# Performance work log

Measured on AMD Instinct MI355X. Metric: run time of the kernel, lower is better.

Reference implementation:

```python
import jax, jax.numpy as jnp
import numpy as np

B, T = 64, 512
N_EMB, HIDDEN, VOCAB = 768, 256, 3072


def setup_inputs() -> dict:
    key = jax.random.key(0)
    ks = jax.random.split(key, 5)
    def xavier(k, shape):
        bound = float(np.sqrt(6.0 / (shape[0] + shape[1])))
        return jax.random.uniform(k, shape, jnp.float32, -bound, bound)
    return {
        "idx": jax.random.randint(ks[0], (B, T), 0, VOCAB),
        "emb_table": jax.random.normal(ks[1], (VOCAB, N_EMB), jnp.float32),
        "Wxh": xavier(ks[2], (N_EMB, HIDDEN)),
        "Whh": xavier(ks[3], (HIDDEN, HIDDEN)),
        "Wy": xavier(ks[4], (HIDDEN, VOCAB)),
        "By": jnp.zeros((VOCAB,), jnp.float32),
        "Bh": jnp.zeros((HIDDEN,), jnp.float32),
    }


def reference(idx, emb_table, Wxh, Whh, Wy, By, Bh):
    # embedded: [B, T, E] -> scan over time with hidden carry [B, H]
    embedded = emb_table[idx]                      # gather
    xWxh = jnp.einsum('bte,eh->tbh', embedded, Wxh)  # precompute input projection

    def step(hidden, x_t):
        hidden = jnp.tanh(x_t + hidden @ Whh + Bh)
        return hidden, None

    h0 = jnp.zeros((idx.shape[0], Whh.shape[0]), embedded.dtype)
    hidden, _ = jax.lax.scan(step, h0, xWxh)
    # return_sequences=False: only the last step's output is returned
    out = hidden @ Wy + By
    return out, hidden
```

## Files before the change

### kernel.cpp

```cpp
#include <hip/hip_runtime.h>
#include <hip/hip_bf16.h>

typedef _Float16 half8 __attribute__((ext_vector_type(8)));
typedef float f32x4 __attribute__((ext_vector_type(4)));

#define B_SZ 64
#define T_SZ 512
#define E_SZ 768
#define H_SZ 256
#define V_SZ 3072

#define WS_P     0u
#define WS_WT    16777216u
#define WS_WF    17170432u

static __device__ __forceinline__ float fast_tanh(float x) {
  float e = __builtin_amdgcn_exp2f(x * 2.8853900817779268f);
  return 1.0f - 2.0f * __builtin_amdgcn_rcpf(1.0f + e);
}

__global__ __launch_bounds__(256) void k0_convert(
    const float* __restrict__ Wxh,
    const float* __restrict__ Whh,
    _Float16* __restrict__ Wtf,
    _Float16* __restrict__ Wf)
{
  int gid = blockIdx.x * 256 + threadIdx.x;
  if (gid < E_SZ * H_SZ) {
    int e = gid >> 8, n = gid & 255;
    float v = Wxh[gid];
    int ki = e >> 5, kb = (e >> 3) & 3, j = e & 7;
    int f  = ((n >> 4) << 6) | (kb << 4) | (n & 15);
    Wtf[(size_t)ki * 8192 + (size_t)f * 8 + j] = (_Float16)v;
  }
  if (gid < 65536) {
    int row = gid >> 8, col = gid & 255;
    float v = Whh[gid];
    int kt = row >> 5, quad = (row >> 3) & 3, j = row & 7;
    int nt = col >> 4;
    int lane = (quad << 4) | (col & 15);
    Wf[(((size_t)(nt * 8 + kt) * 64 + lane) * 8) + j] = (_Float16)v;
  }
}

__global__ __launch_bounds__(256) void k1_xproj(
    const float* __restrict__ emb,
    const _Float16* __restrict__ Wtf,
    _Float16* __restrict__ P)
{
  const int tid  = threadIdx.x;
  const int w    = tid >> 6;
  const int lane = tid & 63;
  const int m16  = lane & 15;
  const int quad = lane >> 4;
  const int r = blockIdx.x * 64 + w * 16 + m16;
  const float* Arow = emb + (size_t)r * E_SZ + quad * 8;

  __shared__ __align__(16) _Float16 bp[2][16 * 64 * 8];
  uint4 stg[4];
#pragma unroll
  for (int pp = 0; pp < 4; ++pp)
    stg[pp] = *(const uint4*)(Wtf + (size_t)(tid + 256 * pp) * 8);
  f32x4 af0 = *(const f32x4*)(Arow);
  f32x4 af1 = *(const f32x4*)(Arow + 4);

  f32x4 acc[16];
#pragma unroll
  for (int n = 0; n < 16; ++n) { f32x4 z = {0.f, 0.f, 0.f, 0.f}; acc[n] = z; }

#pragma unroll
  for (int pp = 0; pp < 4; ++pp)
    *(uint4*)(bp[0] + (size_t)(tid + 256 * pp) * 8) = stg[pp];
  __syncthreads();

#pragma unroll 1
  for (int ki = 0; ki < 24; ++ki) {
    const _Float16* cur = bp[ki & 1];
    f32x4 af0n = af0, af1n = af1;
    if (ki < 23) {
#pragma unroll
      for (int pp = 0; pp < 4; ++pp)
        stg[pp] = *(const uint4*)(Wtf + (size_t)(ki + 1) * 8192
                                      + (size_t)(tid + 256 * pp) * 8);
      af0n = *(const f32x4*)(Arow + (ki + 1) * 32);
      af1n = *(const f32x4*)(Arow + (ki + 1) * 32 + 4);
    }
    half8 a;
#pragma unroll
    for (int e = 0; e < 4; ++e) { a[e] = (_Float16)af0[e]; a[4 + e] = (_Float16)af1[e]; }
#pragma unroll
    for (int nt = 0; nt < 16; ++nt) {
      half8 bb = *(const half8*)(cur + (size_t)(nt * 64 + lane) * 8);
      acc[nt] = __builtin_amdgcn_mfma_f32_16x16x32_f16(a, bb, acc[nt], 0, 0, 0);
    }
    if (ki < 23) {
#pragma unroll
      for (int pp = 0; pp < 4; ++pp)
        *(uint4*)(bp[(ki + 1) & 1] + (size_t)(tid + 256 * pp) * 8) = stg[pp];
      __syncthreads();
    }
    af0 = af0n; af1 = af1n;
  }
  const int rbase = blockIdx.x * 64 + w * 16 + quad * 4;
#pragma unroll
  for (int nt = 0; nt < 16; ++nt) {
    const int col = nt * 16 + m16;
#pragma unroll
    for (int rg = 0; rg < 4; ++rg) {
      P[(size_t)(rbase + rg) * H_SZ + col] = (_Float16)acc[nt][rg];
    }
  }
}

#define LDFRAG(C, KT, R0, R1, R2, R3) { \
  uint4 q = Wf4[(((size_t)(w * 4 + C) * 8 + KT) * 64) + lane]; \
  asm volatile("v_accvgpr_write_b32 a" #R0 ", %0" :: "v"(q.x) : "a" #R0); \
  asm volatile("v_accvgpr_write_b32 a" #R1 ", %0" :: "v"(q.y) : "a" #R1); \
  asm volatile("v_accvgpr_write_b32 a" #R2 ", %0" :: "v"(q.z) : "a" #R2); \
  asm volatile("v_accvgpr_write_b32 a" #R3 ", %0" :: "v"(q.w) : "a" #R3); }

#define MFMA_K0(A0, Z) \
  asm volatile( \
    "v_mfma_f32_16x16x32_f16 %[t0], %[a], a[0:3],   %[z]\n\t" \
    "v_mfma_f32_16x16x32_f16 %[t1], %[a], a[32:35], %[z]\n\t" \
    "v_mfma_f32_16x16x32_f16 %[t2], %[a], a[64:67], %[z]\n\t" \
    "v_mfma_f32_16x16x32_f16 %[t3], %[a], a[96:99], %[z]" \
    : [t0] "=&v"(acc0), [t1] "=&v"(acc1), [t2] "=&v"(acc2), [t3] "=&v"(acc3) \
    : [a] "v"(A0), [z] "v"(Z));

#define MFMA_KT(A0, B0, B1, B2, B3) \
  asm volatile( \
    "v_mfma_f32_16x16x32_f16 %[t0], %[a], a[" #B0 "], %[t0]\n\t" \
    "v_mfma_f32_16x16x32_f16 %[t1], %[a], a[" #B1 "], %[t1]\n\t" \
    "v_mfma_f32_16x16x32_f16 %[t2], %[a], a[" #B2 "], %[t2]\n\t" \
    "v_mfma_f32_16x16x32_f16 %[t3], %[a], a[" #B3 "], %[t3]" \
    : [t0] "+v"(acc0), [t1] "+v"(acc1), [t2] "+v"(acc2), [t3] "+v"(acc3) \
    : [a] "v"(A0));

#define MFMA_K7(A0, B0, B1, B2, B3) \
  asm volatile( \
    "v_mfma_f32_16x16x32_f16 %[t0], %[a], a[" #B0 "], %[t0]\n\t" \
    "v_mfma_f32_16x16x32_f16 %[t1], %[a], a[" #B1 "], %[t1]\n\t" \
    "v_mfma_f32_16x16x32_f16 %[t2], %[a], a[" #B2 "], %[t2]\n\t" \
    "v_mfma_f32_16x16x32_f16 %[t3], %[a], a[" #B3 "], %[t3]\n\t" \
    "s_nop 7\n\t" \
    "s_nop 7" \
    : [t0] "+v"(acc0), [t1] "+v"(acc1), [t2] "+v"(acc2), [t3] "+v"(acc3) \
    : [a] "v"(A0));

__global__ __launch_bounds__(256) void k2_rnn(
    const _Float16* __restrict__ Wf,
    const _Float16* __restrict__ P,
    const int* __restrict__ idx,
    const float* __restrict__ Bh,
    const float* __restrict__ Wy,
    const float* __restrict__ By,
    float* __restrict__ out,
    float* __restrict__ hidout)
{
  const int b    = blockIdx.x;
  const int tid  = threadIdx.x;
  const int w    = tid >> 6;
  const int lane = tid & 63;
  const int quad = lane >> 4;
  __shared__ __align__(16) _Float16 hb[2][H_SZ];
  __shared__ int   ids[520];
  __shared__ float hf[H_SZ];
  const uint4* Wf4 = (const uint4*)Wf;

  LDFRAG(0,0,  0,  1,  2,  3)  LDFRAG(0,1,  4,  5,  6,  7)
  LDFRAG(0,2,  8,  9, 10, 11)  LDFRAG(0,3, 12, 13, 14, 15)
  LDFRAG(0,4, 16, 17, 18, 19)  LDFRAG(0,5, 20, 21, 22, 23)
  LDFRAG(0,6, 24, 25, 26, 27)  LDFRAG(0,7, 28, 29, 30, 31)
  LDFRAG(1,0, 32, 33, 34, 35)  LDFRAG(1,1, 36, 37, 38, 39)
  LDFRAG(1,2, 40, 41, 42, 43)  LDFRAG(1,3, 44, 45, 46, 47)
  LDFRAG(1,4, 48, 49, 50, 51)  LDFRAG(1,5, 52, 53, 54, 55)
  LDFRAG(1,6, 56, 57, 58, 59)  LDFRAG(1,7, 60, 61, 62, 63)
  LDFRAG(2,0, 64, 65, 66, 67)  LDFRAG(2,1, 68, 69, 70, 71)
  LDFRAG(2,2, 72, 73, 74, 75)  LDFRAG(2,3, 76, 77, 78, 79)
  LDFRAG(2,4, 80, 81, 82, 83)  LDFRAG(2,5, 84, 85, 86, 87)
  LDFRAG(2,6, 88, 89, 90, 91)  LDFRAG(2,7, 92, 93, 94, 95)
  LDFRAG(3,0, 96, 97, 98, 99)  LDFRAG(3,1,100,101,102,103)
  LDFRAG(3,2,104,105,106,107)  LDFRAG(3,3,108,109,110,111)
  LDFRAG(3,4,112,113,114,115)  LDFRAG(3,5,116,117,118,119)
  LDFRAG(3,6,120,121,122,123)  LDFRAG(3,7,124,125,126,127)

  const float bhj = Bh[tid];
  const int* idxb = idx + b * T_SZ;
  for (int i = tid; i < 520; i += 256) ids[i] = idxb[i < 512 ? i : 511];
  int rowA = idxb[2];
  int rowB = idxb[3];
  _Float16 xA = P[(size_t)idxb[0] * H_SZ + tid];
  _Float16 xB = P[(size_t)idxb[1] * H_SZ + tid];
  f32x4 zero4 = {0.f, 0.f, 0.f, 0.f};
  asm volatile("" : "+v"(zero4));
  hb[1][tid] = (_Float16)0.f;
  float hval = 0.f;
  __syncthreads();

#define K2_STEP(HR, HW, XV)                                              \
  {                                                                      \
    const _Float16* hr = (HR);                                           \
    half8 va0 = *(const half8*)(hr +   0 + quad * 8);                    \
    half8 va1 = *(const half8*)(hr +  32 + quad * 8);                    \
    half8 va2 = *(const half8*)(hr +  64 + quad * 8);                    \
    half8 va3 = *(const half8*)(hr +  96 + quad * 8);                    \
    half8 va4 = *(const half8*)(hr + 128 + quad * 8);                    \
    half8 va5 = *(const half8*)(hr + 160 + quad * 8);                    \
    half8 va6 = *(const half8*)(hr + 192 + quad * 8);                    \
    half8 va7 = *(const half8*)(hr + 224 + quad * 8);                    \
    f32x4 acc0, acc1, acc2, acc3;                                        \
    MFMA_K0(va0, zero4)                                                  \
    MFMA_KT(va1,   4:7,  36:39,  68:71, 100:103)                         \
    MFMA_KT(va2,  8:11,  40:43,  72:75, 104:107)                         \
    MFMA_KT(va3, 12:15,  44:47,  76:79, 108:111)                         \
    MFMA_KT(va4, 16:19,  48:51,  80:83, 112:115)                         \
    MFMA_KT(va5, 20:23,  52:55,  84:87, 116:119)                         \
    MFMA_KT(va6, 24:27,  56:59,  88:91, 120:123)                         \
    MFMA_K7(va7, 28:31,  60:63,  92:95, 124:127)                         \
    float v0 = acc0[0], v1 = acc1[0], v2 = acc2[0], v3 = acc3[0];        \
    float ylo = (quad & 1) ? v1 : v0;                                    \
    float yhi = (quad & 1) ? v3 : v2;                                    \
    float y   = (quad & 2) ? yhi : ylo;          \
    hval = fast_tanh(y + (XV) + bhj);                                    \
    (HW)[tid] = (_Float16)hval;                                          \
    __syncthreads();                                                     \
  }

#pragma unroll 1
  for (int tt = 0; tt < 256; ++tt) {
    float xvA = (float)xA;
    xA = P[rowA * H_SZ + tid];
    rowA = ids[2 * tt + 4];
    K2_STEP(hb[1], hb[0], xvA)
    float xvB = (float)xB;
    xB = P[rowB * H_SZ + tid];
    rowB = ids[2 * tt + 5];
    K2_STEP(hb[0], hb[1], xvB)
  }
#undef K2_STEP
  hidout[b * H_SZ + tid] = hval;

  hf[tid] = hval;
  __syncthreads();
#pragma unroll 1
  for (int c = 0; c < 12; ++c) {
    const int v = c * 256 + tid;
    float a0 = By[v], a1 = 0.f, a2 = 0.f, a3 = 0.f;
#pragma unroll 4
    for (int jj = 0; jj < H_SZ; jj += 4) {
      a0 += hf[jj + 0] * Wy[(size_t)(jj + 0) * V_SZ + v];
      a1 += hf[jj + 1] * Wy[(size_t)(jj + 1) * V_SZ + v];
      a2 += hf[jj + 2] * Wy[(size_t)(jj + 2) * V_SZ + v];
      a3 += hf[jj + 3] * Wy[(size_t)(jj + 3) * V_SZ + v];
    }
    out[(size_t)b * V_SZ + v] = (a0 + a1) + (a2 + a3);
  }
}

extern "C" void kernel_launch(void* const* d_in, const int* in_sizes, int n_in,
                              void* d_out, int out_size, void* d_ws, size_t ws_size,
                              hipStream_t stream)
{
  const int*   idx = (const int*)d_in[0];
  const float* emb = (const float*)d_in[1];
  const float* Wxh = (const float*)d_in[2];
  const float* Whh = (const float*)d_in[3];
  const float* Wy  = (const float*)d_in[4];
  const float* By  = (const float*)d_in[5];
  const float* Bh  = (const float*)d_in[6];

  char* ws = (char*)d_ws;
  _Float16* P    = (_Float16*)(ws + WS_P);
  _Float16* Wtf  = (_Float16*)(ws + WS_WT);
  _Float16* Wf   = (_Float16*)(ws + WS_WF);

  float* out    = (float*)d_out;
  float* hidout = out + (size_t)B_SZ * V_SZ;

  k0_convert<<<768, 256, 0, stream>>>(Wxh, Whh, Wtf, Wf);
  k1_xproj  <<<48, 256, 0, stream>>>(emb, Wtf, P);
  k2_rnn    <<<64, 256, 0, stream>>>(Wf, P, idx, Bh, Wy, By, out, hidout);
}
```

Measured before the change: 403.7 us.

## Fuse weight conversion into projection kernel and restructure output GEMV loop

Merges the weight-conversion and vocabulary-projection kernels into one launch. Extra blocks convert Whh, while the projection blocks read and convert Wxh panels from fp32 on the fly, so the intermediate Wtf buffer is no longer written and reread. The RNN kernel drops the shared-memory index staging in favour of direct global reads of idx with clamping. The final output GEMV is reordered so each thread keeps 12 accumulators and loads each hidden value once per row pair. The trade-off is strided, uncoalesced fp32 reads of Wxh inside the projection loop and extra global index loads in the serial recurrence.

```diff
diff --git a/kernel.cpp b/kernel.cpp
--- a/kernel.cpp
+++ b/kernel.cpp
@@ -11,44 +11,35 @@
 #define V_SZ 3072
 
 #define WS_P     0u
-#define WS_WT    16777216u
-#define WS_WF    17170432u
+#define WS_WF    1572864u
 
 static __device__ __forceinline__ float fast_tanh(float x) {
   float e = __builtin_amdgcn_exp2f(x * 2.8853900817779268f);
   return 1.0f - 2.0f * __builtin_amdgcn_rcpf(1.0f + e);
 }
 
-__global__ __launch_bounds__(256) void k0_convert(
+__global__ __launch_bounds__(256) void k01(
+    const float* __restrict__ emb,
     const float* __restrict__ Wxh,
     const float* __restrict__ Whh,
-    _Float16* __restrict__ Wtf,
+    _Float16* __restrict__ P,
     _Float16* __restrict__ Wf)
 {
-  int gid = blockIdx.x * 256 + threadIdx.x;
-  if (gid < E_SZ * H_SZ) {
-    int e = gid >> 8, n = gid & 255;
-    float v = Wxh[gid];
-    int ki = e >> 5, kb = (e >> 3) & 3, j = e & 7;
-    int f  = ((n >> 4) << 6) | (kb << 4) | (n & 15);
-    Wtf[(size_t)ki * 8192 + (size_t)f * 8 + j] = (_Float16)v;
-  }
-  if (gid < 65536) {
-    int row = gid >> 8, col = gid & 255;
-    float v = Whh[gid];
-    int kt = row >> 5, quad = (row >> 3) & 3, j = row & 7;
-    int nt = col >> 4;
-    int lane = (quad << 4) | (col & 15);
-    Wf[(((size_t)(nt * 8 + kt) * 64 + lane) * 8) + j] = (_Float16)v;
-  }
-}
-
-__global__ __launch_bounds__(256) void k1_xproj(
-    const float* __restrict__ emb,
-    const _Float16* __restrict__ Wtf,
-    _Float16* __restrict__ P)
-{
-  const int tid  = threadIdx.x;
+  const int tid = threadIdx.x;
+  if (blockIdx.x >= 48) {
+    const int base = (blockIdx.x - 48) * 1024;
+#pragma unroll
+    for (int k = 0; k < 4; ++k) {
+      const int g0 = base + k * 256 + tid;
+      const int row = g0 >> 8, col = g0 & 255;
+      const float v = Whh[g0];
+      const int kt = row >> 5, quad = (row >> 3) & 3, j = row & 7;
+      const int nt = col >> 4;
+      const int lane = (quad << 4) | (col & 15);
+      Wf[(((size_t)(nt * 8 + kt) * 64 + lane) * 8) + j] = (_Float16)v;
+    }
+    return;
+  }
   const int w    = tid >> 6;
   const int lane = tid & 63;
   const int m16  = lane & 15;
@@ -57,10 +48,35 @@
   const float* Arow = emb + (size_t)r * E_SZ + quad * 8;
 
   __shared__ __align__(16) _Float16 bp[2][16 * 64 * 8];
-  uint4 stg[4];
-#pragma unroll
-  for (int pp = 0; pp < 4; ++pp)
-    stg[pp] = *(const uint4*)(Wtf + (size_t)(tid + 256 * pp) * 8);
+
+  int n_[4], kb_[4];
+#pragma unroll
+  for (int pp = 0; pp < 4; ++pp) {
+    int f = tid + 256 * pp;
+    n_[pp]  = ((f >> 6) << 4) | (f & 15);
+    kb_[pp] = (f >> 4) & 3;
+  }
+
+  f32x4 s0[4], s1[4];
+#define LOADPAN(KI) { \
+  _Pragma("unroll") \
+  for (int pp = 0; pp < 4; ++pp) { \
+    const float* src = Wxh + (size_t)((KI) * 32 + kb_[pp] * 8) * H_SZ + n_[pp]; \
+    s0[pp][0] = src[0 * H_SZ]; s0[pp][1] = src[1 * H_SZ]; \
+    s0[pp][2] = src[2 * H_SZ]; s0[pp][3] = src[3 * H_SZ]; \
+    s1[pp][0] = src[4 * H_SZ]; s1[pp][1] = src[5 * H_SZ]; \
+    s1[pp][2] = src[6 * H_SZ]; s1[pp][3] = src[7 * H_SZ]; \
+  } }
+#define WRITEPAN(BUF) { \
+  _Pragma("unroll") \
+  for (int pp = 0; pp < 4; ++pp) { \
+    half8 hh; \
+    _Pragma("unroll") \
+    for (int j = 0; j < 4; ++j) { hh[j] = (_Float16)s0[pp][j]; hh[4 + j] = (_Float16)s1[pp][j]; } \
+    *(half8*)(bp[BUF] + (size_t)(tid + 256 * pp) * 8) = hh; \
+  } }
+
+  LOADPAN(0)
   f32x4 af0 = *(const f32x4*)(Arow);
   f32x4 af1 = *(const f32x4*)(Arow + 4);
 
@@ -68,9 +84,7 @@
 #pragma unroll
   for (int n = 0; n < 16; ++n) { f32x4 z = {0.f, 0.f, 0.f, 0.f}; acc[n] = z; }
 
-#pragma unroll
-  for (int pp = 0; pp < 4; ++pp)
-    *(uint4*)(bp[0] + (size_t)(tid + 256 * pp) * 8) = stg[pp];
+  WRITEPAN(0)
   __syncthreads();
 
 #pragma unroll 1
@@ -78,10 +92,7 @@
     const _Float16* cur = bp[ki & 1];
     f32x4 af0n = af0, af1n = af1;
     if (ki < 23) {
-#pragma unroll
-      for (int pp = 0; pp < 4; ++pp)
-        stg[pp] = *(const uint4*)(Wtf + (size_t)(ki + 1) * 8192
-                                      + (size_t)(tid + 256 * pp) * 8);
+      LOADPAN(ki + 1)
       af0n = *(const f32x4*)(Arow + (ki + 1) * 32);
       af1n = *(const f32x4*)(Arow + (ki + 1) * 32 + 4);
     }
@@ -94,9 +105,7 @@
       acc[nt] = __builtin_amdgcn_mfma_f32_16x16x32_f16(a, bb, acc[nt], 0, 0, 0);
     }
     if (ki < 23) {
-#pragma unroll
-      for (int pp = 0; pp < 4; ++pp)
-        *(uint4*)(bp[(ki + 1) & 1] + (size_t)(tid + 256 * pp) * 8) = stg[pp];
+      WRITEPAN((ki + 1) & 1)
       __syncthreads();
     }
     af0 = af0n; af1 = af1n;
@@ -110,6 +119,8 @@
       P[(size_t)(rbase + rg) * H_SZ + col] = (_Float16)acc[nt][rg];
     }
   }
+#undef LOADPAN
+#undef WRITEPAN
 }
 
 #define LDFRAG(C, KT, R0, R1, R2, R3) { \
@@ -164,7 +175,6 @@
   const int lane = tid & 63;
   const int quad = lane >> 4;
   __shared__ __align__(16) _Float16 hb[2][H_SZ];
-  __shared__ int   ids[520];
   __shared__ float hf[H_SZ];
   const uint4* Wf4 = (const uint4*)Wf;
 
@@ -187,7 +197,6 @@
 
   const float bhj = Bh[tid];
   const int* idxb = idx + b * T_SZ;
-  for (int i = tid; i < 520; i += 256) ids[i] = idxb[i < 512 ? i : 511];
   int rowA = idxb[2];
   int rowB = idxb[3];
   _Float16 xA = P[(size_t)idxb[0] * H_SZ + tid];
@@ -230,12 +239,14 @@
 #pragma unroll 1
   for (int tt = 0; tt < 256; ++tt) {
     float xvA = (float)xA;
-    xA = P[rowA * H_SZ + tid];
-    rowA = ids[2 * tt + 4];
+    xA = P[(size_t)rowA * H_SZ + tid];
+    int t4 = 2 * tt + 4; t4 = t4 > 511 ? 511 : t4;
+    rowA = idxb[t4];
     K2_STEP(hb[1], hb[0], xvA)
     float xvB = (float)xB;
-    xB = P[rowB * H_SZ + tid];
-    rowB = ids[2 * tt + 5];
+    xB = P[(size_t)rowB * H_SZ + tid];
+    int t5 = 2 * tt + 5; t5 = t5 > 511 ? 511 : t5;
+    rowB = idxb[t5];
     K2_STEP(hb[0], hb[1], xvB)
   }
 #undef K2_STEP
@@ -243,19 +254,23 @@
 
   hf[tid] = hval;
   __syncthreads();
+  float oacc[12];
+#pragma unroll
+  for (int c = 0; c < 12; ++c) oacc[c] = By[c * 256 + tid];
 #pragma unroll 1
-  for (int c = 0; c < 12; ++c) {
-    const int v = c * 256 + tid;
-    float a0 = By[v], a1 = 0.f, a2 = 0.f, a3 = 0.f;
-#pragma unroll 4
-    for (int jj = 0; jj < H_SZ; jj += 4) {
-      a0 += hf[jj + 0] * Wy[(size_t)(jj + 0) * V_SZ + v];
-      a1 += hf[jj + 1] * Wy[(size_t)(jj + 1) * V_SZ + v];
-      a2 += hf[jj + 2] * Wy[(size_t)(jj + 2) * V_SZ + v];
-      a3 += hf[jj + 3] * Wy[(size_t)(jj + 3) * V_SZ + v];
-    }
-    out[(size_t)b * V_SZ + v] = (a0 + a1) + (a2 + a3);
-  }
+  for (int jj = 0; jj < H_SZ; jj += 2) {
+    float h0 = hf[jj], h1 = hf[jj + 1];
+    const float* r0 = Wy + (size_t)jj * V_SZ + tid;
+    const float* r1 = r0 + V_SZ;
+#pragma unroll
+    for (int c = 0; c < 12; ++c) {
+      oacc[c] += h0 * r0[c * 256];
+      oacc[c] += h1 * r1[c * 256];
+    }
+  }
+#pragma unroll
+  for (int c = 0; c < 12; ++c)
+    out[(size_t)b * V_SZ + c * 256 + tid] = oacc[c];
 }
 
 extern "C" void kernel_launch(void* const* d_in, const int* in_sizes, int n_in,
@@ -271,14 +286,12 @@
   const float* Bh  = (const float*)d_in[6];
 
   char* ws = (char*)d_ws;
-  _Float16* P    = (_Float16*)(ws + WS_P);
-  _Float16* Wtf  = (_Float16*)(ws + WS_WT);
-  _Float16* Wf   = (_Float16*)(ws + WS_WF);
+  _Float16* P  = (_Float16*)(ws + WS_P);
+  _Float16* Wf = (_Float16*)(ws + WS_WF);
 
   float* out    = (float*)d_out;
   float* hidout = out + (size_t)B_SZ * V_SZ;
 
-  k0_convert<<<768, 256, 0, stream>>>(Wxh, Whh, Wtf, Wf);
-  k1_xproj  <<<48, 256, 0, stream>>>(emb, Wtf, P);
-  k2_rnn    <<<64, 256, 0, stream>>>(Wf, P, idx, Bh, Wy, By, out, hidout);
-}
+  k01   <<<112, 256, 0, stream>>>(emb, Wxh, Whh, P, Wf);
+  k2_rnn<<<64, 256, 0, stream>>>(Wf, P, idx, Bh, Wy, By, out, hidout);
+}
```

Result: faster. 382.9 us (-5.1%).
